# Kernel optimization log

Hardware: AMD Instinct MI355X
Metric: run time of the kernel (lower is better)

The kernel has to match this reference:

```python
import jax, jax.numpy as jnp
import numpy as np

N, E, F, H, HEADS, L, G, NC = 50000, 800000, 128, 64, 4, 3, 64, 2
EPS = 1e-5


def _init(key, shape, fan_in):
    return jax.random.normal(key, shape, jnp.float32) / np.sqrt(fan_in)


def setup_inputs() -> dict:
    key = jax.random.key(0)
    ks = jax.random.split(key, 24)
    x = jax.random.normal(ks[0], (N, F), jnp.float32)
    edge_index = jax.random.randint(ks[1], (2, E), 0, N, jnp.int32)
    batch = jnp.sort(jax.random.randint(ks[2], (N,), 0, G, jnp.int32))
    return {
        "x": x, "edge_index": edge_index, "batch": batch,
        "Wi": _init(ks[3], (F, H), F), "bi": jnp.zeros((H,), jnp.float32),
        "gcn_W": _init(ks[4], (L, H, H), H), "gcn_b": jnp.zeros((L, H), jnp.float32),
        "gcn_gamma": jnp.ones((L, H), jnp.float32), "gcn_beta": jnp.zeros((L, H), jnp.float32),
        "Wg": _init(ks[5], (H, HEADS * H), H), "bg": jnp.zeros((H,), jnp.float32),
        "att_src": _init(ks[6], (HEADS, H), H), "att_dst": _init(ks[7], (HEADS, H), H),
        "gat_gamma": jnp.ones((H,), jnp.float32), "gat_beta": jnp.zeros((H,), jnp.float32),
        "c1_W": _init(ks[8], (2 * H, H), 2 * H), "c1_b": jnp.zeros((H,), jnp.float32),
        "c2_W": _init(ks[9], (H, H // 2), H), "c2_b": jnp.zeros((H // 2,), jnp.float32),
        "c3_W": _init(ks[10], (H // 2, NC), H // 2), "c3_b": jnp.zeros((NC,), jnp.float32),
    }


def _batch_norm(x, gamma, beta):
    # training-mode BN over the node dimension
    mu = x.mean(0)
    var = x.var(0)
    return (x - mu) * jax.lax.rsqrt(var + EPS) * gamma + beta


def _gcn_conv(x, W, b, src, dst):
    # PyG GCNConv: add self loops + symmetric normalization D^-1/2 (A+I) D^-1/2
    h = x @ W  # [N, H]
    ones = jnp.ones((src.shape[0],), h.dtype)
    deg = jax.ops.segment_sum(ones, dst, num_segments=N) + 1.0  # +1 for self loop
    dinv = jax.lax.rsqrt(deg)
    norm = dinv[src] * dinv[dst]  # [E]
    out = jax.ops.segment_sum(h[src] * norm[:, None], dst, num_segments=N)
    out = out + h * (dinv * dinv)[:, None]  # self-loop term: deg^-1
    return out + b


def _gat_conv(x, W, att_s, att_d, b, src, dst):
    # PyG GATConv, concat=False (mean over heads), leaky_relu slope 0.2, self loops
    h = (x @ W).reshape(N, HEADS, H)  # [N, Hd, C]
    a_s = (h * att_s).sum(-1)  # [N, Hd]
    a_d = (h * att_d).sum(-1)
    sl = jnp.arange(N, dtype=src.dtype)
    si = jnp.concatenate([src, sl])
    di = jnp.concatenate([dst, sl])
    logits = jax.nn.leaky_relu(a_s[si] + a_d[di], 0.2)  # [E+N, Hd]
    # segment softmax over destination node per head
    m = jax.ops.segment_max(logits, di, num_segments=N)  # every node has a self loop
    e = jnp.exp(logits - m[di])
    s = jax.ops.segment_sum(e, di, num_segments=N)
    alpha = e / (s[di] + 1e-16)  # [E+N, Hd]
    out = jax.ops.segment_sum(h[si] * alpha[:, :, None], di, num_segments=N)  # [N, Hd, C]
    return out.mean(axis=1) + b


def reference(x, edge_index, batch, Wi, bi, gcn_W, gcn_b, gcn_gamma, gcn_beta,
              Wg, bg, att_src, att_dst, gat_gamma, gat_beta,
              c1_W, c1_b, c2_W, c2_b, c3_W, c3_b):
    src, dst = edge_index[0], edge_index[1]
    h = jax.nn.relu(x @ Wi + bi)
    for l in range(L):
        identity = h
        h = _gcn_conv(h, gcn_W[l], gcn_b[l], src, dst)
        h = _batch_norm(h, gcn_gamma[l], gcn_beta[l])
        h = jax.nn.relu(h)  # dropout: eval mode (identity)
        h = h + identity
    identity = h
    h = _gat_conv(h, Wg, att_src, att_dst, bg, src, dst)
    h = _batch_norm(h, gat_gamma, gat_beta)
    h = jax.nn.elu(h)
    h = h + identity
    # dual pooling over graphs
    cnt = jax.ops.segment_sum(jnp.ones((N,), h.dtype), batch, num_segments=G,
                              indices_are_sorted=True)
    x_mean = jax.ops.segment_sum(h, batch, num_segments=G, indices_are_sorted=True)
    x_mean = x_mean / jnp.maximum(cnt, 1.0)[:, None]
    x_max = jax.ops.segment_max(h, batch, num_segments=G, indices_are_sorted=True)
    x_max = jnp.where(jnp.isfinite(x_max), x_max, 0.0)
    z = jnp.concatenate([x_mean, x_max], axis=1)  # [G, 2H]
    z = jax.nn.relu(z @ c1_W + c1_b)
    z = jax.nn.relu(z @ c2_W + c2_b)
    return z @ c3_W + c3_b  # [G, NC]
```

## Files before the change

kernel.cpp:

```cpp
#include <hip/hip_runtime.h>
#include <math.h>

#define N_ 50000
#define E_ 800000
#define F_ 128
#define H_ 64
#define G_ 64
#define NC_ 2
#define CAP_ 96
#define EPS_ 1e-5f
#define GRID_P 1250
#define GRID_G 2048
#define GRID_W 768
#define WIS_STRIDE 136
#define W0_STRIDE 72
#define WGS 72

typedef _Float16 f16;
typedef f16 f16x2 __attribute__((ext_vector_type(2)));
typedef f16 f16x4 __attribute__((ext_vector_type(4)));
typedef f16 f16x8 __attribute__((ext_vector_type(8)));

__device__ __forceinline__ unsigned fkey(float f) {
    unsigned u = __float_as_uint(f);
    return (u & 0x80000000u) ? ~u : (u | 0x80000000u);
}
__device__ __forceinline__ float funkey(unsigned k) {
    unsigned u = (k & 0x80000000u) ? (k & 0x7fffffffu) : ~k;
    return __uint_as_float(u);
}
__device__ __forceinline__ float leaky(float x) { return x > 0.f ? x : 0.2f * x; }

__device__ __forceinline__ void dot8(const f16x8 w, const f16x8 v,
                                     float& a0, float& a1, float& a2, float& a3) {
    a0 = __builtin_amdgcn_fdot2(__builtin_shufflevector(w, w, 0, 1),
                                __builtin_shufflevector(v, v, 0, 1), a0, false);
    a1 = __builtin_amdgcn_fdot2(__builtin_shufflevector(w, w, 2, 3),
                                __builtin_shufflevector(v, v, 2, 3), a1, false);
    a2 = __builtin_amdgcn_fdot2(__builtin_shufflevector(w, w, 4, 5),
                                __builtin_shufflevector(v, v, 4, 5), a2, false);
    a3 = __builtin_amdgcn_fdot2(__builtin_shufflevector(w, w, 6, 7),
                                __builtin_shufflevector(v, v, 6, 7), a3, false);
}

__device__ __forceinline__ int sel4(int4 v, int i) {
    return i == 0 ? v.x : i == 1 ? v.y : i == 2 ? v.z : v.w;
}

__global__ void k_fill(const int* __restrict__ ei, int* __restrict__ rowcnt,
                       int* __restrict__ slotS) {
    int e = blockIdx.x * 256 + threadIdx.x;
    if (e >= E_) return;
    int d = ei[E_ + e];
    int pos = atomicAdd(&rowcnt[d], 1);
    if (pos < CAP_) slotS[d * CAP_ + pos] = ei[e];
}

__global__ __launch_bounds__(256) void k_in_mm(const float* __restrict__ x,
                                               const float* __restrict__ Wi,
                                               const float* __restrict__ bi,
                                               const float* __restrict__ W0,
                                               const int* __restrict__ rowcnt,
                                               float* __restrict__ hA,
                                               f16* __restrict__ hWs) {
    __shared__ __attribute__((aligned(16))) f16 Wis[H_ * WIS_STRIDE];
    __shared__ __attribute__((aligned(16))) f16 W0s[H_ * W0_STRIDE];
    __shared__ __attribute__((aligned(16))) f16 xb[4 * F_];
    __shared__ __attribute__((aligned(16))) f16 rb[4 * H_];
    int tid = threadIdx.x;
    for (int i = tid; i < F_ * H_; i += 256) {
        int k = i >> 6, j = i & 63;
        Wis[j * WIS_STRIDE + k] = (f16)Wi[i];
    }
    for (int i = tid; i < H_ * H_; i += 256) {
        int k = i >> 6, j = i & 63;
        W0s[j * W0_STRIDE + k] = (f16)W0[i];
    }
    __syncthreads();
    int r = tid >> 6, j = tid & 63;
    float bj = bi[j];
    const f16* wc1 = Wis + j * WIS_STRIDE;
    const f16* wc2 = W0s + j * W0_STRIDE;
    f16* xr = xb + r * F_;
    f16* rr = rb + r * H_;
    int grp = blockIdx.x;
    float2 xv = *(const float2*)&x[(size_t)(grp * 4 + r) * F_ + 2 * j];
    for (; grp < N_ / 4; grp += GRID_P) {
        f16x2 xs = {(f16)xv.x, (f16)xv.y};
        *(f16x2*)&xr[2 * j] = xs;
        int ng = grp + GRID_P;
        if (ng < N_ / 4)
            xv = *(const float2*)&x[(size_t)(ng * 4 + r) * F_ + 2 * j];
        int n = grp * 4 + r;
        float a0 = 0.f, a1 = 0.f, a2 = 0.f, a3 = 0.f;
#pragma unroll
        for (int k = 0; k < F_; k += 8)
            dot8(*(const f16x8*)&wc1[k], *(const f16x8*)&xr[k], a0, a1, a2, a3);
        float y = fmaxf((a0 + a1) + (a2 + a3) + bj, 0.f);
        hA[(size_t)n * H_ + j] = y;
        rr[j] = (f16)y;
        float b0 = 0.f, b1 = 0.f, b2 = 0.f, b3 = 0.f;
#pragma unroll
        for (int k = 0; k < H_; k += 8)
            dot8(*(const f16x8*)&wc2[k], *(const f16x8*)&rr[k], b0, b1, b2, b3);
        hWs[(size_t)n * H_ + j] =
            (f16)(((b0 + b1) + (b2 + b3)) * rsqrtf((float)rowcnt[n] + 1.f));
    }
}

__global__ __launch_bounds__(256) void k_gcn_gather(const int* __restrict__ rowcnt,
                                                    const int* __restrict__ slotS,
                                                    const f16* __restrict__ hWs,
                                                    float* __restrict__ out,
                                                    float* __restrict__ bnpart) {
    __shared__ float st[128];
    for (int i = threadIdx.x; i < 128; i += 256) st[i] = 0.f;
    __syncthreads();
    int L = threadIdx.x & 63;
    int rg = L >> 4, q = L & 15;
    for (int grp = blockIdx.x; grp < N_ / 4; grp += GRID_G) {
        int d = grp * 4 + (threadIdx.x >> 6);
        int rc = rowcnt[d];
        int cnt = min(rc, CAP_);
        float dd = rsqrtf((float)rc + 1.f);
        size_t base = (size_t)d * CAP_;
        float a0 = 0.f, a1 = 0.f, a2 = 0.f, a3 = 0.f;
        if (rg == 0) {
            f16x4 hv = *(const f16x4*)&hWs[(size_t)d * H_ + q * 4];
            a0 = (float)hv[0]; a1 = (float)hv[1]; a2 = (float)hv[2]; a3 = (float)hv[3];
        }
        for (int k = 0; k < cnt; k += 16) {
            int4 iA = *(const int4*)&slotS[base + k];
            int4 iB = *(const int4*)&slotS[base + k + 4];
            int4 iC = *(const int4*)&slotS[base + k + 8];
            int4 iD = *(const int4*)&slotS[base + k + 12];
            int e = k + rg;
            int s0 = (e < cnt) ? sel4(iA, rg) : d;
            int s1 = (e + 4 < cnt) ? sel4(iB, rg) : d;
            int s2 = (e + 8 < cnt) ? sel4(iC, rg) : d;
            int s3 = (e + 12 < cnt) ? sel4(iD, rg) : d;
            f16x4 v0 = *(const f16x4*)&hWs[(size_t)s0 * H_ + q * 4];
            f16x4 v1 = *(const f16x4*)&hWs[(size_t)s1 * H_ + q * 4];
            f16x4 v2 = *(const f16x4*)&hWs[(size_t)s2 * H_ + q * 4];
            f16x4 v3 = *(const f16x4*)&hWs[(size_t)s3 * H_ + q * 4];
            float m0 = (e < cnt) ? 1.f : 0.f;
            float m1 = (e + 4 < cnt) ? 1.f : 0.f;
            float m2 = (e + 8 < cnt) ? 1.f : 0.f;
            float m3 = (e + 12 < cnt) ? 1.f : 0.f;
            a0 += (m0 * (float)v0[0] + m1 * (float)v1[0]) +
                  (m2 * (float)v2[0] + m3 * (float)v3[0]);
            a1 += (m0 * (float)v0[1] + m1 * (float)v1[1]) +
                  (m2 * (float)v2[1] + m3 * (float)v3[1]);
            a2 += (m0 * (float)v0[2] + m1 * (float)v1[2]) +
                  (m2 * (float)v2[2] + m3 * (float)v3[2]);
            a3 += (m0 * (float)v0[3] + m1 * (float)v1[3]) +
                  (m2 * (float)v2[3] + m3 * (float)v3[3]);
        }
        a0 += __shfl_xor(a0, 16); a0 += __shfl_xor(a0, 32);
        a1 += __shfl_xor(a1, 16); a1 += __shfl_xor(a1, 32);
        a2 += __shfl_xor(a2, 16); a2 += __shfl_xor(a2, 32);
        a3 += __shfl_xor(a3, 16); a3 += __shfl_xor(a3, 32);
        if (rg == 0) {
            float y0 = a0 * dd, y1 = a1 * dd, y2 = a2 * dd, y3 = a3 * dd;
            *(float4*)&out[(size_t)d * H_ + q * 4] = make_float4(y0, y1, y2, y3);
            atomicAdd(&st[q * 4 + 0], y0);        atomicAdd(&st[64 + q * 4 + 0], y0 * y0);
            atomicAdd(&st[q * 4 + 1], y1);        atomicAdd(&st[64 + q * 4 + 1], y1 * y1);
            atomicAdd(&st[q * 4 + 2], y2);        atomicAdd(&st[64 + q * 4 + 2], y2 * y2);
            atomicAdd(&st[q * 4 + 3], y3);        atomicAdd(&st[64 + q * 4 + 3], y3 * y3);
        }
    }
    __syncthreads();
    for (int i = threadIdx.x; i < 128; i += 256)
        atomicAdd(&bnpart[(blockIdx.x & 255) * 128 + i], st[i]);
}

__global__ void k_bn_final(const float* __restrict__ part, float* __restrict__ stat) {
    int t = threadIdx.x;
    float s = 0.f;
    for (int b = 0; b < 256; b++) s += part[b * 128 + t];
    __shared__ float red[128];
    red[t] = s;
    __syncthreads();
    if (t < H_) {
        float mu = red[t] / (float)N_;
        float var = red[H_ + t] / (float)N_ - mu * mu;
        stat[t] = mu;
        stat[H_ + t] = rsqrtf(var + EPS_);
    }
}

__global__ __launch_bounds__(256) void k_bn_mm(const float* __restrict__ v,
                                               const float* __restrict__ stat,
                                               const float* __restrict__ gamma,
                                               const float* __restrict__ beta,
                                               const float* __restrict__ res,
                                               const float* __restrict__ W,
                                               const int* __restrict__ rowcnt,
                                               float* __restrict__ out_res,
                                               f16* __restrict__ hWs) {
    __shared__ __attribute__((aligned(16))) f16 Ws[H_ * W0_STRIDE];
    __shared__ __attribute__((aligned(16))) f16 rb[4 * H_];
    int tid = threadIdx.x;
    for (int i = tid; i < H_ * H_; i += 256) {
        int k = i >> 6, j = i & 63;
        Ws[j * W0_STRIDE + k] = (f16)W[i];
    }
    __syncthreads();
    int r = tid >> 6, j = tid & 63;
    float mu = stat[j], rs = stat[H_ + j], ga = gamma[j], be = beta[j];
    const f16* wc = Ws + j * W0_STRIDE;
    f16* rr = rb + r * H_;
    for (int grp = blockIdx.x; grp < N_ / 4; grp += GRID_P) {
        int n = grp * 4 + r;
        size_t idx = (size_t)n * H_ + j;
        float y = (v[idx] - mu) * rs * ga + be;
        y = fmaxf(y, 0.f) + res[idx];
        out_res[idx] = y;
        rr[j] = (f16)y;
        float b0 = 0.f, b1 = 0.f, b2 = 0.f, b3 = 0.f;
#pragma unroll
        for (int k = 0; k < H_; k += 8)
            dot8(*(const f16x8*)&wc[k], *(const f16x8*)&rr[k], b0, b1, b2, b3);
        hWs[idx] = (f16)(((b0 + b1) + (b2 + b3)) * rsqrtf((float)rowcnt[n] + 1.f));
    }
}

__global__ __launch_bounds__(256) void k_wg(const float* __restrict__ v,
                                            const float* __restrict__ stat,
                                            const float* __restrict__ gamma,
                                            const float* __restrict__ beta,
                                            const float* __restrict__ res,
                                            const float* __restrict__ Wg,
                                            const float* __restrict__ asw,
                                            const float* __restrict__ adw,
                                            float* __restrict__ hOut,
                                            f16* __restrict__ hg16,
                                            float* __restrict__ a_s,
                                            float* __restrict__ a_d) {
    __shared__ __attribute__((aligned(16))) f16 Wgs[256 * WGS];
    __shared__ __attribute__((aligned(16))) f16 xb[32 * H_];
    int tid = threadIdx.x;
    for (int i = tid; i < H_ * 256; i += 256) {
        int k = i >> 8, j = i & 255;
        Wgs[j * WGS + k] = (f16)Wg[i];
    }
    int c = tid & 63;
    float mu = stat[c], rs = stat[H_ + c], ga = gamma[c], be = beta[c];
    int j = tid, wid = j >> 6, lane = j & 63;
    float aw = asw[j], dw = adw[j];
    const f16* wcol = &Wgs[j * WGS];
    const int NGRP = (N_ + 31) / 32;
    for (int g0 = blockIdx.x; g0 < NGRP; g0 += GRID_W) {
        int n0 = g0 * 32;
        int nrows = min(32, N_ - n0);
        __syncthreads();
        for (int i = tid; i < nrows * H_; i += 256) {
            size_t idx = (size_t)n0 * H_ + i;
            float y = (v[idx] - mu) * rs * ga + be;
            y = fmaxf(y, 0.f) + res[idx];
            hOut[idx] = y;
            xb[i] = (f16)y;
        }
        __syncthreads();
        for (int nn = 0; nn < nrows; nn++) {
            const f16* hr = xb + nn * H_;
            float a0 = 0.f, a1 = 0.f, a2 = 0.f, a3 = 0.f;
#pragma unroll
            for (int k = 0; k < H_; k += 8)
                dot8(*(const f16x8*)&wcol[k], *(const f16x8*)&hr[k], a0, a1, a2, a3);
            float acc = (a0 + a1) + (a2 + a3);
            int n = n0 + nn;
            hg16[(size_t)n * 256 + j] = (f16)acc;
            float ps = acc * aw, pd = acc * dw;
            for (int m = 1; m < 64; m <<= 1) {
                ps += __shfl_xor(ps, m);
                pd += __shfl_xor(pd, m);
            }
            if (lane == 0) { a_s[n * 4 + wid] = ps; a_d[n * 4 + wid] = pd; }
        }
    }
}

__global__ __launch_bounds__(256) void k_gat(const int* __restrict__ rowcnt,
                                             const int* __restrict__ slotS,
                                             const f16* __restrict__ hg16,
                                             const float* __restrict__ a_s,
                                             const float* __restrict__ a_d,
                                             float* __restrict__ out,
                                             float* __restrict__ bnpart) {
    __shared__ float st[4][128];
    int r = threadIdx.x >> 6;
    int d = blockIdx.x * 4 + r;
    int L = threadIdx.x & 63;
    int rg = L >> 5, p = L & 31;
    int h = p >> 3, o = p & 7;
    int cnt = min(rowcnt[d], CAP_);
    size_t base = (size_t)d * CAP_;
    float ads = a_d[d * 4 + h];
    float es = __expf(fminf(leaky(a_s[d * 4 + h] + ads), 19.f) - 8.f);
    float s = 0.f;
    float acc[8];
#pragma unroll
    for (int i = 0; i < 8; i++) acc[i] = 0.f;
    if (rg == 0) {
        s = es;
        f16x8 hv = *(const f16x8*)&hg16[(size_t)d * 256 + p * 8];
#pragma unroll
        for (int i = 0; i < 8; i++) acc[i] = es * (float)hv[i];
    }
    int k = 0;
    for (; k + 8 <= cnt; k += 8) {
        int4 sA = *(const int4*)&slotS[base + k];
        int4 sB = *(const int4*)&slotS[base + k + 4];
        int s0 = rg ? sA.y : sA.x;
        int s1 = rg ? sA.w : sA.z;
        int s2 = rg ? sB.y : sB.x;
        int s3 = rg ? sB.w : sB.z;
        float x0 = a_s[s0 * 4 + h];
        float x1 = a_s[s1 * 4 + h];
        float x2 = a_s[s2 * 4 + h];
        float x3 = a_s[s3 * 4 + h];
        f16x8 v0 = *(const f16x8*)&hg16[(size_t)s0 * 256 + p * 8];
        f16x8 v1 = *(const f16x8*)&hg16[(size_t)s1 * 256 + p * 8];
        f16x8 v2 = *(const f16x8*)&hg16[(size_t)s2 * 256 + p * 8];
        f16x8 v3 = *(const f16x8*)&hg16[(size_t)s3 * 256 + p * 8];
        float t0 = __expf(fminf(leaky(x0 + ads), 19.f) - 8.f);
        float t1 = __expf(fminf(leaky(x1 + ads), 19.f) - 8.f);
        float t2 = __expf(fminf(leaky(x2 + ads), 19.f) - 8.f);
        float t3 = __expf(fminf(leaky(x3 + ads), 19.f) - 8.f);
        s += (t0 + t1) + (t2 + t3);
#pragma unroll
        for (int i = 0; i < 8; i++)
            acc[i] += (t0 * (float)v0[i] + t1 * (float)v1[i]) +
                      (t2 * (float)v2[i] + t3 * (float)v3[i]);
    }
    for (; k < cnt; k += 2) {
        if (k + rg < cnt) {
            int sE = slotS[base + k + rg];
            float t = __expf(fminf(leaky(a_s[sE * 4 + h] + ads), 19.f) - 8.f);
            f16x8 v = *(const f16x8*)&hg16[(size_t)sE * 256 + p * 8];
            s += t;
#pragma unroll
            for (int i = 0; i < 8; i++) acc[i] += t * (float)v[i];
        }
    }
    s += __shfl_xor(s, 32);
#pragma unroll
    for (int i = 0; i < 8; i++) acc[i] += __shfl_xor(acc[i], 32);
    float w = 0.25f / (s + 1e-16f);
#pragma unroll
    for (int i = 0; i < 8; i++) acc[i] *= w;
#pragma unroll
    for (int i = 0; i < 8; i++) {
        acc[i] += __shfl_xor(acc[i], 8);
        acc[i] += __shfl_xor(acc[i], 16);
    }
    if (L < 8) {
        float4 oA = make_float4(acc[0], acc[1], acc[2], acc[3]);
        float4 oB = make_float4(acc[4], acc[5], acc[6], acc[7]);
        *(float4*)&out[(size_t)d * H_ + o * 8] = oA;
        *(float4*)&out[(size_t)d * H_ + o * 8 + 4] = oB;
#pragma unroll
        for (int i = 0; i < 8; i++) {
            st[r][o * 8 + i] = acc[i];
            st[r][64 + o * 8 + i] = acc[i] * acc[i];
        }
    }
    __syncthreads();
    for (int t = threadIdx.x; t < 128; t += 256) {
        float vsum = (st[0][t] + st[1][t]) + (st[2][t] + st[3][t]);
        atomicAdd(&bnpart[(blockIdx.x & 255) * 128 + t], vsum);
    }
}

__global__ __launch_bounds__(256) void k_pool_bn(const float* __restrict__ accv,
                                                 const float* __restrict__ stat,
                                                 const float* __restrict__ gamma,
                                                 const float* __restrict__ beta,
                                                 const float* __restrict__ res,
                                                 const int* __restrict__ batch,
                                                 float* __restrict__ xmean,
                                                 unsigned int* __restrict__ xmaxb,
                                                 float* __restrict__ cnt) {
    const int CH = 196;
    int n0 = blockIdx.x * CH;
    int nEnd = min(n0 + CH, N_);
    int c = threadIdx.x & 63, r = threadIdx.x >> 6;
    float mu = stat[c], rs = stat[H_ + c], ga = gamma[c], be = beta[c];
    int curg = -1, cc = 0;
    float s = 0.f;
    unsigned mk = 0u;
    for (int n = n0 + r; n < nEnd; n += 4) {
        int g = batch[n];
        if (g != curg) {
            if (curg >= 0) {
                atomicAdd(&xmean[curg * H_ + c], s);
                atomicMax(&xmaxb[curg * H_ + c], mk);
                if (c == 0) atomicAdd(&cnt[curg], (float)cc);
            }
            curg = g; s = 0.f; mk = 0u; cc = 0;
        }
        size_t idx = (size_t)n * H_ + c;
        float y = (accv[idx] - mu) * rs * ga + be;
        y = (y > 0.f ? y : expf(y) - 1.f) + res[idx];
        s += y;
        unsigned kv = fkey(y);
        mk = mk > kv ? mk : kv;
        cc++;
    }
    if (curg >= 0) {
        atomicAdd(&xmean[curg * H_ + c], s);
        atomicMax(&xmaxb[curg * H_ + c], mk);
        if (c == 0) atomicAdd(&cnt[curg], (float)cc);
    }
}

__global__ __launch_bounds__(64) void k_head(const float* __restrict__ xmean,
                                             const unsigned int* __restrict__ xmaxb,
                                             const float* __restrict__ cnt,
                                             const float* __restrict__ c1W, const float* __restrict__ c1b,
                                             const float* __restrict__ c2W, const float* __restrict__ c2b,
                                             const float* __restrict__ c3W, const float* __restrict__ c3b,
                                             float* __restrict__ out) {
    __shared__ float z[2 * H_];
    __shared__ float o1[H_];
    __shared__ float o2[32];
    int g = blockIdx.x, j = threadIdx.x;
    float cn = fmaxf(cnt[g], 1.f);
    z[j] = xmean[g * H_ + j] / cn;
    unsigned key = xmaxb[g * H_ + j];
    z[H_ + j] = (key == 0u) ? 0.f : funkey(key);
    __syncthreads();
    float a0 = c1b[j], a1 = 0.f, a2 = 0.f, a3 = 0.f;
    for (int k = 0; k < 2 * H_; k += 4) {
        a0 += z[k] * c1W[k * 64 + j];
        a1 += z[k + 1] * c1W[(k + 1) * 64 + j];
        a2 += z[k + 2] * c1W[(k + 2) * 64 + j];
        a3 += z[k + 3] * c1W[(k + 3) * 64 + j];
    }
    o1[j] = fmaxf((a0 + a1) + (a2 + a3), 0.f);
    __syncthreads();
    if (j < 32) {
        float b0 = c2b[j], b1 = 0.f, b2 = 0.f, b3 = 0.f;
        for (int k = 0; k < H_; k += 4) {
            b0 += o1[k] * c2W[k * 32 + j];
            b1 += o1[k + 1] * c2W[(k + 1) * 32 + j];
            b2 += o1[k + 2] * c2W[(k + 2) * 32 + j];
            b3 += o1[k + 3] * c2W[(k + 3) * 32 + j];
        }
        o2[j] = fmaxf((b0 + b1) + (b2 + b3), 0.f);
    }
    __syncthreads();
    if (j < NC_) {
        float c0 = c3b[j];
        for (int k = 0; k < 32; k++) c0 += o2[k] * c3W[k * 2 + j];
        out[g * NC_ + j] = c0;
    }
}

extern "C" void kernel_launch(void* const* d_in, const int* in_sizes, int n_in,
                              void* d_out, int out_size, void* d_ws, size_t ws_size,
                              hipStream_t stream) {
    const float* x     = (const float*)d_in[0];
    const int*   ei    = (const int*)d_in[1];
    const int*   batch = (const int*)d_in[2];
    const float* Wi    = (const float*)d_in[3];
    const float* bi    = (const float*)d_in[4];
    const float* gcnW  = (const float*)d_in[5];
    const float* gcnG  = (const float*)d_in[7];
    const float* gcnB  = (const float*)d_in[8];
    const float* Wg    = (const float*)d_in[9];
    const float* attS  = (const float*)d_in[11];
    const float* attD  = (const float*)d_in[12];
    const float* gatG  = (const float*)d_in[13];
    const float* gatB  = (const float*)d_in[14];
    const float* c1W   = (const float*)d_in[15];
    const float* c1b   = (const float*)d_in[16];
    const float* c2W   = (const float*)d_in[17];
    const float* c2b   = (const float*)d_in[18];
    const float* c3W   = (const float*)d_in[19];
    const float* c3b   = (const float*)d_in[20];
    float* out = (float*)d_out;

    float* p = (float*)d_ws;
    float* hA    = p; p += (size_t)N_ * H_;
    float* hB    = p; p += (size_t)N_ * H_;
    float* acc   = p; p += (size_t)N_ * H_;
    f16*   hg16  = (f16*)p; p += (size_t)N_ * 128;
    float* a_s   = p; p += (size_t)N_ * 4;
    float* a_d   = p; p += (size_t)N_ * 4;
    float* bnstat = p; p += 2 * H_;
    float* xmean  = p; p += G_ * H_;
    unsigned int* xmaxb = (unsigned int*)p; p += G_ * H_;
    float* cnt = p; p += G_;
    int* rowcnt = (int*)p; p += N_;
    float* bnpart4 = p; p += 4 * 256 * 128;
    int* slotS = (int*)p; p += (size_t)N_ * CAP_ + 16;
    f16* hWs = (f16*)hg16;

    float* bnp0 = bnpart4;
    float* bnp1 = bnpart4 + 1 * 256 * 128;
    float* bnp2 = bnpart4 + 2 * 256 * 128;
    float* bnp3 = bnpart4 + 3 * 256 * 128;

    const int NB_E = (E_ + 255) / 256;
    const int NB_W = N_ / 4;

    hipMemsetAsync(rowcnt, 0, (N_ + 4 * 256 * 128) * sizeof(float), stream);
    k_fill<<<NB_E, 256, 0, stream>>>(ei, rowcnt, slotS);

    k_in_mm<<<GRID_P, 256, 0, stream>>>(x, Wi, bi, gcnW, rowcnt, hA, hWs);

    k_gcn_gather<<<GRID_G, 256, 0, stream>>>(rowcnt, slotS, hWs, acc, bnp0);
    k_bn_final<<<1, 128, 0, stream>>>(bnp0, bnstat);
    k_bn_mm<<<GRID_P, 256, 0, stream>>>(acc, bnstat, gcnG, gcnB, hA,
                                        gcnW + (size_t)1 * H_ * H_, rowcnt, hB, hWs);
    k_gcn_gather<<<GRID_G, 256, 0, stream>>>(rowcnt, slotS, hWs, acc, bnp1);
    k_bn_final<<<1, 128, 0, stream>>>(bnp1, bnstat);
    k_bn_mm<<<GRID_P, 256, 0, stream>>>(acc, bnstat, gcnG + H_, gcnB + H_, hB,
                                        gcnW + (size_t)2 * H_ * H_, rowcnt, hA, hWs);
    k_gcn_gather<<<GRID_G, 256, 0, stream>>>(rowcnt, slotS, hWs, acc, bnp2);
    k_bn_final<<<1, 128, 0, stream>>>(bnp2, bnstat);

    k_wg<<<GRID_W, 256, 0, stream>>>(acc, bnstat, gcnG + 2 * H_, gcnB + 2 * H_,
                                     hA, Wg, attS, attD, hB, hg16, a_s, a_d);
    k_gat<<<NB_W, 256, 0, stream>>>(rowcnt, slotS, hg16, a_s, a_d, acc, bnp3);
    k_bn_final<<<1, 128, 0, stream>>>(bnp3, bnstat);

    hipMemsetAsync(xmean, 0, (G_ * H_ * 2 + G_) * sizeof(float), stream);
    k_pool_bn<<<256, 256, 0, stream>>>(acc, bnstat, gatG, gatB, hB, batch,
                                       xmean, xmaxb, cnt);

    k_head<<<G_, 64, 0, stream>>>(xmean, xmaxb, cnt, c1W, c1b, c2W, c2b, c3W, c3b, out);
}
```

Before: 529.6 us.

## Use one-block-per-group launches for GCN gather and GAT projection kernels

The GCN gather and Wg projection kernels drop their grid-stride loops and launch one block per 4-node group (gather) or per 32-row tile (projection). The gather kernel's inner loop is rewritten to process 8 neighbours per step without masking, with a scalar tail loop. Its per-block BN statistics now go through a per-row shared array reduced once, replacing shared atomics. The cost is more blocks, and each projection block now reloads and converts the full Wg matrix into shared memory.

```diff
diff --git a/kernel.cpp b/kernel.cpp
--- a/kernel.cpp
+++ b/kernel.cpp
@@ -10,8 +10,6 @@
 #define CAP_ 96
 #define EPS_ 1e-5f
 #define GRID_P 1250
-#define GRID_G 2048
-#define GRID_W 768
 #define WIS_STRIDE 136
 #define W0_STRIDE 72
 #define WGS 72
@@ -113,65 +111,58 @@
                                                     const f16* __restrict__ hWs,
                                                     float* __restrict__ out,
                                                     float* __restrict__ bnpart) {
-    __shared__ float st[128];
-    for (int i = threadIdx.x; i < 128; i += 256) st[i] = 0.f;
-    __syncthreads();
+    __shared__ float st[4][128];
+    int r = threadIdx.x >> 6;
+    int d = blockIdx.x * 4 + r;
     int L = threadIdx.x & 63;
     int rg = L >> 4, q = L & 15;
-    for (int grp = blockIdx.x; grp < N_ / 4; grp += GRID_G) {
-        int d = grp * 4 + (threadIdx.x >> 6);
-        int rc = rowcnt[d];
-        int cnt = min(rc, CAP_);
-        float dd = rsqrtf((float)rc + 1.f);
-        size_t base = (size_t)d * CAP_;
-        float a0 = 0.f, a1 = 0.f, a2 = 0.f, a3 = 0.f;
-        if (rg == 0) {
-            f16x4 hv = *(const f16x4*)&hWs[(size_t)d * H_ + q * 4];
-            a0 = (float)hv[0]; a1 = (float)hv[1]; a2 = (float)hv[2]; a3 = (float)hv[3];
-        }
-        for (int k = 0; k < cnt; k += 16) {
-            int4 iA = *(const int4*)&slotS[base + k];
-            int4 iB = *(const int4*)&slotS[base + k + 4];
-            int4 iC = *(const int4*)&slotS[base + k + 8];
-            int4 iD = *(const int4*)&slotS[base + k + 12];
-            int e = k + rg;
-            int s0 = (e < cnt) ? sel4(iA, rg) : d;
-            int s1 = (e + 4 < cnt) ? sel4(iB, rg) : d;
-            int s2 = (e + 8 < cnt) ? sel4(iC, rg) : d;
-            int s3 = (e + 12 < cnt) ? sel4(iD, rg) : d;
-            f16x4 v0 = *(const f16x4*)&hWs[(size_t)s0 * H_ + q * 4];
-            f16x4 v1 = *(const f16x4*)&hWs[(size_t)s1 * H_ + q * 4];
-            f16x4 v2 = *(const f16x4*)&hWs[(size_t)s2 * H_ + q * 4];
-            f16x4 v3 = *(const f16x4*)&hWs[(size_t)s3 * H_ + q * 4];
-            float m0 = (e < cnt) ? 1.f : 0.f;
-            float m1 = (e + 4 < cnt) ? 1.f : 0.f;
-            float m2 = (e + 8 < cnt) ? 1.f : 0.f;
-            float m3 = (e + 12 < cnt) ? 1.f : 0.f;
-            a0 += (m0 * (float)v0[0] + m1 * (float)v1[0]) +
-                  (m2 * (float)v2[0] + m3 * (float)v3[0]);
-            a1 += (m0 * (float)v0[1] + m1 * (float)v1[1]) +
-                  (m2 * (float)v2[1] + m3 * (float)v3[1]);
-            a2 += (m0 * (float)v0[2] + m1 * (float)v1[2]) +
-                  (m2 * (float)v2[2] + m3 * (float)v3[2]);
-            a3 += (m0 * (float)v0[3] + m1 * (float)v1[3]) +
-                  (m2 * (float)v2[3] + m3 * (float)v3[3]);
-        }
-        a0 += __shfl_xor(a0, 16); a0 += __shfl_xor(a0, 32);
-        a1 += __shfl_xor(a1, 16); a1 += __shfl_xor(a1, 32);
-        a2 += __shfl_xor(a2, 16); a2 += __shfl_xor(a2, 32);
-        a3 += __shfl_xor(a3, 16); a3 += __shfl_xor(a3, 32);
-        if (rg == 0) {
-            float y0 = a0 * dd, y1 = a1 * dd, y2 = a2 * dd, y3 = a3 * dd;
-            *(float4*)&out[(size_t)d * H_ + q * 4] = make_float4(y0, y1, y2, y3);
-            atomicAdd(&st[q * 4 + 0], y0);        atomicAdd(&st[64 + q * 4 + 0], y0 * y0);
-            atomicAdd(&st[q * 4 + 1], y1);        atomicAdd(&st[64 + q * 4 + 1], y1 * y1);
-            atomicAdd(&st[q * 4 + 2], y2);        atomicAdd(&st[64 + q * 4 + 2], y2 * y2);
-            atomicAdd(&st[q * 4 + 3], y3);        atomicAdd(&st[64 + q * 4 + 3], y3 * y3);
-        }
-    }
-    __syncthreads();
-    for (int i = threadIdx.x; i < 128; i += 256)
-        atomicAdd(&bnpart[(blockIdx.x & 255) * 128 + i], st[i]);
+    int rc = rowcnt[d];
+    int cnt = min(rc, CAP_);
+    float dd = rsqrtf((float)rc + 1.f);
+    size_t base = (size_t)d * CAP_;
+    float a0 = 0.f, a1 = 0.f, a2 = 0.f, a3 = 0.f;
+    if (rg == 0) {
+        f16x4 hv = *(const f16x4*)&hWs[(size_t)d * H_ + q * 4];
+        a0 = (float)hv[0]; a1 = (float)hv[1]; a2 = (float)hv[2]; a3 = (float)hv[3];
+    }
+    int k = 0;
+    for (; k + 8 <= cnt; k += 8) {
+        int4 sA = *(const int4*)&slotS[base + k];
+        int4 sB = *(const int4*)&slotS[base + k + 4];
+        int s0 = sel4(sA, rg);
+        int s1 = sel4(sB, rg);
+        f16x4 v0 = *(const f16x4*)&hWs[(size_t)s0 * H_ + q * 4];
+        f16x4 v1 = *(const f16x4*)&hWs[(size_t)s1 * H_ + q * 4];
+        a0 += (float)v0[0] + (float)v1[0];
+        a1 += (float)v0[1] + (float)v1[1];
+        a2 += (float)v0[2] + (float)v1[2];
+        a3 += (float)v0[3] + (float)v1[3];
+    }
+    for (; k < cnt; k += 4) {
+        if (k + rg < cnt) {
+            int s = slotS[base + k + rg];
+            f16x4 v = *(const f16x4*)&hWs[(size_t)s * H_ + q * 4];
+            a0 += (float)v[0]; a1 += (float)v[1];
+            a2 += (float)v[2]; a3 += (float)v[3];
+        }
+    }
+    a0 += __shfl_xor(a0, 16); a0 += __shfl_xor(a0, 32);
+    a1 += __shfl_xor(a1, 16); a1 += __shfl_xor(a1, 32);
+    a2 += __shfl_xor(a2, 16); a2 += __shfl_xor(a2, 32);
+    a3 += __shfl_xor(a3, 16); a3 += __shfl_xor(a3, 32);
+    if (rg == 0) {
+        float y0 = a0 * dd, y1 = a1 * dd, y2 = a2 * dd, y3 = a3 * dd;
+        *(float4*)&out[(size_t)d * H_ + q * 4] = make_float4(y0, y1, y2, y3);
+        st[r][q * 4 + 0] = y0;  st[r][64 + q * 4 + 0] = y0 * y0;
+        st[r][q * 4 + 1] = y1;  st[r][64 + q * 4 + 1] = y1 * y1;
+        st[r][q * 4 + 2] = y2;  st[r][64 + q * 4 + 2] = y2 * y2;
+        st[r][q * 4 + 3] = y3;  st[r][64 + q * 4 + 3] = y3 * y3;
+    }
+    __syncthreads();
+    for (int t = threadIdx.x; t < 128; t += 256) {
+        float vsum = (st[0][t] + st[1][t]) + (st[2][t] + st[3][t]);
+        atomicAdd(&bnpart[(blockIdx.x & 255) * 128 + t], vsum);
+    }
 }
 
 __global__ void k_bn_final(const float* __restrict__ part, float* __restrict__ stat) {
@@ -244,16 +235,11 @@
         int k = i >> 8, j = i & 255;
         Wgs[j * WGS + k] = (f16)Wg[i];
     }
-    int c = tid & 63;
-    float mu = stat[c], rs = stat[H_ + c], ga = gamma[c], be = beta[c];
-    int j = tid, wid = j >> 6, lane = j & 63;
-    float aw = asw[j], dw = adw[j];
-    const f16* wcol = &Wgs[j * WGS];
-    const int NGRP = (N_ + 31) / 32;
-    for (int g0 = blockIdx.x; g0 < NGRP; g0 += GRID_W) {
-        int n0 = g0 * 32;
-        int nrows = min(32, N_ - n0);
-        __syncthreads();
+    int n0 = blockIdx.x * 32;
+    int nrows = min(32, N_ - n0);
+    {
+        int c = tid & 63;
+        float mu = stat[c], rs = stat[H_ + c], ga = gamma[c], be = beta[c];
         for (int i = tid; i < nrows * H_; i += 256) {
             size_t idx = (size_t)n0 * H_ + i;
             float y = (v[idx] - mu) * rs * ga + be;
@@ -261,23 +247,26 @@
             hOut[idx] = y;
             xb[i] = (f16)y;
         }
-        __syncthreads();
-        for (int nn = 0; nn < nrows; nn++) {
-            const f16* hr = xb + nn * H_;
-            float a0 = 0.f, a1 = 0.f, a2 = 0.f, a3 = 0.f;
-#pragma unroll
-            for (int k = 0; k < H_; k += 8)
-                dot8(*(const f16x8*)&wcol[k], *(const f16x8*)&hr[k], a0, a1, a2, a3);
-            float acc = (a0 + a1) + (a2 + a3);
-            int n = n0 + nn;
-            hg16[(size_t)n * 256 + j] = (f16)acc;
-            float ps = acc * aw, pd = acc * dw;
-            for (int m = 1; m < 64; m <<= 1) {
-                ps += __shfl_xor(ps, m);
-                pd += __shfl_xor(pd, m);
-            }
-            if (lane == 0) { a_s[n * 4 + wid] = ps; a_d[n * 4 + wid] = pd; }
-        }
+    }
+    __syncthreads();
+    int j = tid, wid = j >> 6, lane = j & 63;
+    float aw = asw[j], dw = adw[j];
+    const f16* wcol = &Wgs[j * WGS];
+    for (int nn = 0; nn < nrows; nn++) {
+        const f16* hr = xb + nn * H_;
+        float a0 = 0.f, a1 = 0.f, a2 = 0.f, a3 = 0.f;
+#pragma unroll
+        for (int k = 0; k < H_; k += 8)
+            dot8(*(const f16x8*)&wcol[k], *(const f16x8*)&hr[k], a0, a1, a2, a3);
+        float acc = (a0 + a1) + (a2 + a3);
+        int n = n0 + nn;
+        hg16[(size_t)n * 256 + j] = (f16)acc;
+        float ps = acc * aw, pd = acc * dw;
+        for (int m = 1; m < 64; m <<= 1) {
+            ps += __shfl_xor(ps, m);
+            pd += __shfl_xor(pd, m);
+        }
+        if (lane == 0) { a_s[n * 4 + wid] = ps; a_d[n * 4 + wid] = pd; }
     }
 }
 
@@ -511,19 +500,19 @@
 
     k_in_mm<<<GRID_P, 256, 0, stream>>>(x, Wi, bi, gcnW, rowcnt, hA, hWs);
 
-    k_gcn_gather<<<GRID_G, 256, 0, stream>>>(rowcnt, slotS, hWs, acc, bnp0);
+    k_gcn_gather<<<NB_W, 256, 0, stream>>>(rowcnt, slotS, hWs, acc, bnp0);
     k_bn_final<<<1, 128, 0, stream>>>(bnp0, bnstat);
     k_bn_mm<<<GRID_P, 256, 0, stream>>>(acc, bnstat, gcnG, gcnB, hA,
                                         gcnW + (size_t)1 * H_ * H_, rowcnt, hB, hWs);
-    k_gcn_gather<<<GRID_G, 256, 0, stream>>>(rowcnt, slotS, hWs, acc, bnp1);
+    k_gcn_gather<<<NB_W, 256, 0, stream>>>(rowcnt, slotS, hWs, acc, bnp1);
     k_bn_final<<<1, 128, 0, stream>>>(bnp1, bnstat);
     k_bn_mm<<<GRID_P, 256, 0, stream>>>(acc, bnstat, gcnG + H_, gcnB + H_, hB,
                                         gcnW + (size_t)2 * H_ * H_, rowcnt, hA, hWs);
-    k_gcn_gather<<<GRID_G, 256, 0, stream>>>(rowcnt, slotS, hWs, acc, bnp2);
+    k_gcn_gather<<<NB_W, 256, 0, stream>>>(rowcnt, slotS, hWs, acc, bnp2);
     k_bn_final<<<1, 128, 0, stream>>>(bnp2, bnstat);
 
-    k_wg<<<GRID_W, 256, 0, stream>>>(acc, bnstat, gcnG + 2 * H_, gcnB + 2 * H_,
-                                     hA, Wg, attS, attD, hB, hg16, a_s, a_d);
+    k_wg<<<(N_ + 31) / 32, 256, 0, stream>>>(acc, bnstat, gcnG + 2 * H_, gcnB + 2 * H_,
+                                             hA, Wg, attS, attD, hB, hg16, a_s, a_d);
     k_gat<<<NB_W, 256, 0, stream>>>(rowcnt, slotS, hg16, a_s, a_d, acc, bnp3);
     k_bn_final<<<1, 128, 0, stream>>>(bnp3, bnstat);
 
```

After: 480.1 us. -9.4%, faster.
